# Performance work log

Measured on AMD Instinct MI355X. Metric: run time of the kernel, lower is better.

The kernel has to match this reference:

```python
import jax, jax.numpy as jnp
import numpy as np

B, L = 512, 260          # batch, raw input length
N_EMB, E_DIM = 8192, 128 * 65
NC = 16                   # num_classes


def setup_inputs() -> dict:
    key = jax.random.key(0)
    ks = jax.random.split(key, 12)
    rn = lambda k, shp, s: jax.random.normal(k, shp, jnp.float32) * s
    return {
        "x": rn(ks[0], (B, L), 1.0),
        # VQ codebook, init uniform(-1/K, 1/K) as in reference VQ-VAE
        "codebook": jax.random.uniform(ks[1], (N_EMB, E_DIM), jnp.float32, -1.0 / N_EMB, 1.0 / N_EMB),
        # encoder: Conv1d(1,64,k4,s2,p1) -> ReLU -> Conv1d(64,128,k4,s2,p1)
        "conv1_w": rn(ks[2], (64, 1, 4), 0.3), "conv1_b": jnp.zeros((64,), jnp.float32),
        "conv2_w": rn(ks[3], (128, 64, 4), 0.06), "conv2_b": jnp.zeros((128,), jnp.float32),
        # decoder: ConvT1d(128,64,k4,s2,p1) -> ReLU -> ConvT1d(64,1,k4,s2,p1); torch weight layout (in,out,k)
        "dec1_w": rn(ks[4], (128, 64, 4), 0.04), "dec1_b": jnp.zeros((64,), jnp.float32),
        "dec2_w": rn(ks[5], (64, 1, 4), 0.06), "dec2_b": jnp.zeros((1,), jnp.float32),
        # multitask head: Linear(4160, NC); torch layout (out,in)
        "mt_w": rn(ks[6], (NC, 4160), 0.015), "mt_b": jnp.zeros((NC,), jnp.float32),
        # adversary head: Linear(4160,256)->ReLU->Linear(256,128)->ReLU->Linear(128,NC)
        "adv_w1": rn(ks[7], (256, 4160), 0.015), "adv_b1": jnp.zeros((256,), jnp.float32),
        "adv_w2": rn(ks[8], (128, 256), 0.06), "adv_b2": jnp.zeros((128,), jnp.float32),
        "adv_w3": rn(ks[9], (NC, 128), 0.09), "adv_b3": jnp.zeros((NC,), jnp.float32),
        "beta": 0.25,
    }


def _conv1d(x, w, b, stride):
    # x: [B,C,L], w: [O,I,K] (torch Conv1d layout), padding=1
    y = jax.lax.conv_general_dilated(x, w, (stride,), [(1, 1)],
                                     dimension_numbers=("NCH", "OIH", "NCH"))
    return y + b[None, :, None]


def _convT1d(x, w, b, stride, k=4, p=1):
    # torch ConvTranspose1d(in,out,k,stride=s,padding=p); w: [I,O,K]
    # == dilated conv with lhs_dilation=s, padding=k-1-p, spatially-flipped, IO-swapped kernel
    wt = jnp.flip(w, -1).transpose(1, 0, 2)  # [O,I,K]
    pad = k - 1 - p
    y = jax.lax.conv_general_dilated(x, wt, (1,), [(pad, pad)], lhs_dilation=(stride,),
                                     dimension_numbers=("NCH", "OIH", "NCH"))
    return y + b[None, :, None]


def _forward(x, codebook, conv1_w, conv1_b, conv2_w, conv2_b,
             dec1_w, dec1_b, dec2_w, dec2_b, mt_w, mt_b,
             adv_w1, adv_b1, adv_w2, adv_b2, adv_w3, adv_b3, beta):
    sg = jax.lax.stop_gradient
    xb = x[:, None, :]                                      # x.unsqueeze_(1) -> [B,1,260]
    h = jax.nn.relu(_conv1d(xb, conv1_w, conv1_b, 2))       # [B,64,130]
    z_e = _conv1d(h, conv2_w, conv2_b, 2)                   # [B,128,65]
    b = z_e.shape[0]

    # ---- VectorQuantizer: cdist^2 / argmin / gather / commitment loss ----
    z = z_e.reshape(b, -1)                                  # [B,8320]
    d = (jnp.sum(z * z, axis=1, keepdims=True)
         + jnp.sum(codebook * codebook, axis=1)[None, :]
         - 2.0 * (z @ codebook.T))                          # [B,N_EMB]
    idx = jnp.argmin(d, axis=1)                             # [B]
    zq_raw = codebook[idx].reshape(z_e.shape)               # gather -> [B,128,65]
    emb_loss = (jnp.mean((sg(zq_raw) - z_e) ** 2)
                + beta * jnp.mean((zq_raw - sg(z_e)) ** 2))
    z_q = z_e + sg(zq_raw - z_e)                            # straight-through
    counts = jnp.zeros((codebook.shape[0],), z.dtype).at[idx].add(1.0)
    e_mean = counts / b
    perplexity = jnp.exp(-jnp.sum(e_mean * jnp.log(e_mean + 1e-10)))

    # ---- heads operate on z_e halves ----
    mt = z_e[:, :64, :].reshape(b, -1) @ mt_w.T + mt_b      # [B,NC]
    a = jax.nn.relu(z_e[:, 64:, :].reshape(b, -1) @ adv_w1.T + adv_b1)
    a = jax.nn.relu(a @ adv_w2.T + adv_b2)
    adv = a @ adv_w3.T + adv_b3                             # [B,NC]

    # ---- decoder on quantized codes ----
    hd = jax.nn.relu(_convT1d(z_q, dec1_w, dec1_b, 2))      # [B,64,130]
    x_hat = _convT1d(hd, dec2_w, dec2_b, 2)                 # [B,1,260]
    return emb_loss, x_hat, mt, adv, perplexity


def reference(x, codebook, conv1_w, conv1_b, conv2_w, conv2_b,
              dec1_w, dec1_b, dec2_w, dec2_b, mt_w, mt_b,
              adv_w1, adv_b1, adv_w2, adv_b2, adv_w3, adv_b3, beta):
    return _forward(x, codebook, conv1_w, conv1_b, conv2_w, conv2_b,
                    dec1_w, dec1_b, dec2_w, dec2_b, mt_w, mt_b,
                    adv_w1, adv_b1, adv_w2, adv_b2, adv_w3, adv_b3, beta)
```

## Files before the change

### kernel.cpp

```cpp
#include <hip/hip_runtime.h>
#include <stdint.h>

typedef __attribute__((ext_vector_type(8))) short s8v;
typedef __attribute__((ext_vector_type(4))) float f4v;

#define OUT_XHAT 1
#define OUT_MT   133121
#define OUT_ADV  141313
#define OUT_PERP 149505

#define WS_COUNTS   0
#define WS_EMB      8192
#define WS_A1       8256
#define WS_CN       139328
#define WS_ZN2      147520
#define WS_ZL1      148032
#define WS_CBL1     148544
#define WS_ZERO_N   156736
#define WS_ZE       156736
#define WS_SC0      4416576
#define WS_SC1      8610880
#define WS_HD       8676416
#define WS_W2T      12936256
#define WS_WE       12969024
#define WS_WO       12985408
#define WS_W2TA     13001792
#define WS_IDX      13034560
#define WS_ZPK      13035136
#define WS_CBT      15165056

__device__ __forceinline__ short f2bf(float f) {
  uint32_t u = __float_as_uint(f);
  u = (u + 0x7FFFu + ((u >> 16) & 1u)) >> 16;
  return (short)u;
}

__device__ __forceinline__ void gl_lds16(const void* g, void* l) {
  __builtin_amdgcn_global_load_lds(
      (const __attribute__((address_space(1))) void*)g,
      (__attribute__((address_space(3))) void*)l, 16, 0, 0);
}

__global__ void k_initprep(float* __restrict__ W, const float* __restrict__ c2w,
                           const float* __restrict__ d1w,
                           const float* __restrict__ aw2) {
  int id = blockIdx.x * 256 + threadIdx.x;
  if (id < WS_ZERO_N) W[id] = 0.f;
  float* w2t = W + WS_W2T;
  float* We = W + WS_WE;
  float* Wo = W + WS_WO;
  float* w2ta = W + WS_W2TA;
  if (id < 32768) {
    int c = id & 127, ik = id >> 7;
    int i = ik >> 2, k = ik & 3;
    w2t[id] = c2w[(c * 64 + i) * 4 + k];
    int kk = id >> 7;
    w2ta[id] = aw2[(id & 127) * 256 + kk];
  }
  if (id < 16384) {
    int o = id & 63, is = id >> 6;
    int i = is >> 1, s = is & 1;
    We[id] = d1w[(i * 64 + o) * 4 + (3 - 2 * s)];
    Wo[id] = d1w[(i * 64 + o) * 4 + (2 - 2 * s)];
  }
}

__device__ __forceinline__ void packmat_body(
    const float* __restrict__ src, short* __restrict__ dst,
    float* __restrict__ nrm2, float* __restrict__ l1, int R, int nb, int bid,
    int tid, short* tile, float* rsq, float* rl1) {
  int n0 = (bid % nb) * 64;
  int k0 = (bid / nb) * 64;
  int nr = tid >> 2, qc = tid & 3;
  const float* sp = src + (size_t)(n0 + nr) * 8320 + k0 + qc * 16;
  float v[16];
  *(float4*)&v[0] = *(const float4*)(sp);
  *(float4*)&v[4] = *(const float4*)(sp + 4);
  *(float4*)&v[8] = *(const float4*)(sp + 8);
  *(float4*)&v[12] = *(const float4*)(sp + 12);
  float sq = 0.f, sl = 0.f;
#pragma unroll
  for (int i = 0; i < 16; ++i) {
    sq = fmaf(v[i], v[i], sq);
    sl += fabsf(v[i]);
  }
  union { short s[8]; int4 q; } u0, u1;
#pragma unroll
  for (int j = 0; j < 8; ++j) {
    u0.s[j] = f2bf(v[j]);
    u1.s[j] = f2bf(v[8 + j]);
  }
  *(int4*)&tile[((qc * 2 + 0) * 64 + nr) * 8] = u0.q;
  *(int4*)&tile[((qc * 2 + 1) * 64 + nr) * 8] = u1.q;
  rsq[tid] = sq;
  rl1[tid] = sl;
  __syncthreads();
  if (tid < 64) {
    float s = rsq[tid * 4] + rsq[tid * 4 + 1] + rsq[tid * 4 + 2] + rsq[tid * 4 + 3];
    float t = rl1[tid * 4] + rl1[tid * 4 + 1] + rl1[tid * 4 + 2] + rl1[tid * 4 + 3];
    atomicAdd(&nrm2[n0 + tid], s);
    atomicAdd(&l1[n0 + tid], t);
  }
  int kc = tid >> 5, nn = (tid & 31) * 2;
  size_t ob = ((size_t)(k0 / 8 + kc) * R + n0 + nn) * 8;
  *(int4*)&dst[ob] = *(int4*)&tile[(kc * 64 + nn) * 8];
  *(int4*)&dst[ob + 8] = *(int4*)&tile[(kc * 64 + nn + 1) * 8];
}

__global__ __launch_bounds__(256) void k_megaA(
    const float* __restrict__ x, const float* __restrict__ c1w,
    const float* __restrict__ c1b, const float* __restrict__ w2t,
    const float* __restrict__ c2b, float* __restrict__ zebuf,
    const float* __restrict__ cb, short* __restrict__ cbt,
    float* __restrict__ cn, float* __restrict__ cbl1) {
  __shared__ __align__(16) char smem[28032];
  int bid = blockIdx.x, tid = threadIdx.x;
  if (bid < 520) {
    float* At = (float*)smem;
    float* Bt = At + 2048;
    float* xs = Bt + 4096;
    float* w1s = xs + 520;
    float* b1s = w1s + 256;
    int row0 = bid * 64;
    int tm = (tid & 15) * 4;
    int tn = (tid >> 4) * 8;
    int sr = tid & 63;
    int sj0 = (tid >> 6) * 8;
    int rowm = row0 + sr;
    int gb = rowm / 65;
    int gt = rowm - gb * 65;
    int gb0 = row0 / 65;
    int xrow = gb - gb0;
    int tpos = 2 * gt - 1;
    int bkr = tid >> 3;
    int bnc = (tid & 7) * 16;
    for (int u = tid; u < 520; u += 256) {
      int rr = gb0 + (u >= 260 ? 1 : 0);
      if (rr > 511) rr = 511;
      xs[u] = x[rr * 260 + (u >= 260 ? u - 260 : u)];
    }
    if (tid < 256) w1s[tid] = c1w[tid];
    if (tid < 64) b1s[tid] = c1b[tid];
    __syncthreads();
    float acc[4][8];
#pragma unroll
    for (int i = 0; i < 4; ++i)
#pragma unroll
      for (int j = 0; j < 8; ++j) acc[i][j] = 0.f;
    for (int k0i = 0; k0i < 256; k0i += 32) {
      float av[8];
#pragma unroll
      for (int u = 0; u < 8; ++u) {
        int jj = k0i + sj0 + u;
        int cc = jj >> 2;
        int kk = jj & 3;
        int p = tpos + kk;
        float hv = 0.f;
        if (p >= 0 && p < 130) {
          float a = b1s[cc];
          int base = 2 * p - 1;
#pragma unroll
          for (int k = 0; k < 4; ++k) {
            int xp = base + k;
            float xv = (xp >= 0 && xp < 260) ? xs[xrow * 260 + xp] : 0.f;
            a = fmaf(xv, w1s[cc * 4 + k], a);
          }
          hv = fmaxf(a, 0.f);
        }
        av[u] = hv;
      }
      float bvv[16];
#pragma unroll
      for (int u = 0; u < 16; ++u) bvv[u] = w2t[(k0i + bkr) * 128 + bnc + u];
      __syncthreads();
#pragma unroll
      for (int u = 0; u < 8; ++u) At[(sj0 + u) * 64 + sr] = av[u];
#pragma unroll
      for (int u = 0; u < 16; ++u) Bt[bkr * 128 + bnc + u] = bvv[u];
      __syncthreads();
#pragma unroll
      for (int kk = 0; kk < 32; ++kk) {
        float a0 = At[kk * 64 + tm + 0];
        float a1 = At[kk * 64 + tm + 1];
        float a2 = At[kk * 64 + tm + 2];
        float a3 = At[kk * 64 + tm + 3];
#pragma unroll
        for (int j = 0; j < 8; ++j) {
          float bv = Bt[kk * 128 + tn + j];
          acc[0][j] = fmaf(a0, bv, acc[0][j]);
          acc[1][j] = fmaf(a1, bv, acc[1][j]);
          acc[2][j] = fmaf(a2, bv, acc[2][j]);
          acc[3][j] = fmaf(a3, bv, acc[3][j]);
        }
      }
    }
#pragma unroll
    for (int i = 0; i < 4; ++i) {
      int rr = row0 + tm + i;
      int b = rr / 65, t = rr - b * 65;
#pragma unroll
      for (int j = 0; j < 8; ++j) {
        int n = tn + j;
        zebuf[(size_t)b * 8320 + (size_t)n * 65 + t] = acc[i][j] + c2b[n];
      }
    }
  } else {
    short* tile = (short*)smem;
    float* rsq = (float*)(smem + 8192);
    float* rl1 = rsq + 256;
    packmat_body(cb, cbt, cn, cbl1, 8192, 128, bid - 520, tid, tile, rsq, rl1);
  }
}

__global__ __launch_bounds__(256) void k_megaB(
    const float* __restrict__ z_e, const float* __restrict__ mtw,
    const float* __restrict__ mtb, const float* __restrict__ aw1,
    short* __restrict__ zpk, float* __restrict__ zn2, float* __restrict__ zl1,
    float* __restrict__ a1, float* __restrict__ out) {
  __shared__ __align__(16) char smem[16384];
  int bid = blockIdx.x, tid = threadIdx.x;
  if (bid < 320) {
    float* At = (float*)smem;
    float* Bt = At + 2048;
    int ksp = bid % 10;
    int nt = (bid / 10) & 3;
    int mt = bid / 40;
    int m0 = mt * 64, n0 = nt * 64, kb = ksp * 416;
    int tm = (tid & 15) * 4, tn = (tid >> 4) * 4;
    int sr = tid & 63, sj = (tid >> 6) * 8;
    const float* za = z_e + (size_t)(m0 + sr) * 8320 + 4160 + kb + sj;
    const float* wb = aw1 + (size_t)(n0 + sr) * 4160 + kb + sj;
    float acc[4][4];
#pragma unroll
    for (int i = 0; i < 4; ++i)
#pragma unroll
      for (int j = 0; j < 4; ++j) acc[i][j] = 0.f;
    for (int k0 = 0; k0 < 416; k0 += 32) {
      float4 av0 = *(const float4*)(za + k0);
      float4 av1 = *(const float4*)(za + k0 + 4);
      float4 bv0 = *(const float4*)(wb + k0);
      float4 bv1 = *(const float4*)(wb + k0 + 4);
      __syncthreads();
      At[(sj + 0) * 64 + sr] = av0.x; At[(sj + 1) * 64 + sr] = av0.y;
      At[(sj + 2) * 64 + sr] = av0.z; At[(sj + 3) * 64 + sr] = av0.w;
      At[(sj + 4) * 64 + sr] = av1.x; At[(sj + 5) * 64 + sr] = av1.y;
      At[(sj + 6) * 64 + sr] = av1.z; At[(sj + 7) * 64 + sr] = av1.w;
      Bt[(sj + 0) * 64 + sr] = bv0.x; Bt[(sj + 1) * 64 + sr] = bv0.y;
      Bt[(sj + 2) * 64 + sr] = bv0.z; Bt[(sj + 3) * 64 + sr] = bv0.w;
      Bt[(sj + 4) * 64 + sr] = bv1.x; Bt[(sj + 5) * 64 + sr] = bv1.y;
      Bt[(sj + 6) * 64 + sr] = bv1.z; Bt[(sj + 7) * 64 + sr] = bv1.w;
      __syncthreads();
#pragma unroll
      for (int kk = 0; kk < 32; ++kk) {
        float4 aa = *(const float4*)&At[kk * 64 + tm];
        float4 bb = *(const float4*)&Bt[kk * 64 + tn];
        acc[0][0] = fmaf(aa.x, bb.x, acc[0][0]); acc[0][1] = fmaf(aa.x, bb.y, acc[0][1]);
        acc[0][2] = fmaf(aa.x, bb.z, acc[0][2]); acc[0][3] = fmaf(aa.x, bb.w, acc[0][3]);
        acc[1][0] = fmaf(aa.y, bb.x, acc[1][0]); acc[1][1] = fmaf(aa.y, bb.y, acc[1][1]);
        acc[1][2] = fmaf(aa.y, bb.z, acc[1][2]); acc[1][3] = fmaf(aa.y, bb.w, acc[1][3]);
        acc[2][0] = fmaf(aa.z, bb.x, acc[2][0]); acc[2][1] = fmaf(aa.z, bb.y, acc[2][1]);
        acc[2][2] = fmaf(aa.z, bb.z, acc[2][2]); acc[2][3] = fmaf(aa.z, bb.w, acc[2][3]);
        acc[3][0] = fmaf(aa.w, bb.x, acc[3][0]); acc[3][1] = fmaf(aa.w, bb.y, acc[3][1]);
        acc[3][2] = fmaf(aa.w, bb.z, acc[3][2]); acc[3][3] = fmaf(aa.w, bb.w, acc[3][3]);
      }
    }
#pragma unroll
    for (int i = 0; i < 4; ++i)
#pragma unroll
      for (int j = 0; j < 4; ++j)
        atomicAdd(&a1[(size_t)(m0 + tm + i) * 256 + n0 + tn + j], acc[i][j]);
  } else if (bid < 832) {
    float* red = (float*)smem;
    int b = bid - 320;
    int wave = tid >> 6, lane = tid & 63;
    const float* zr = z_e + (size_t)b * 8320;
    float acc[16];
#pragma unroll
    for (int n = 0; n < 16; ++n) acc[n] = 0.f;
    for (int k4 = tid; k4 < 1040; k4 += 256) {
      float4 zv = *(const float4*)&zr[k4 * 4];
#pragma unroll
      for (int n = 0; n < 16; ++n) {
        float4 wv = *(const float4*)&mtw[n * 4160 + k4 * 4];
        float a = acc[n];
        a = fmaf(zv.x, wv.x, a);
        a = fmaf(zv.y, wv.y, a);
        a = fmaf(zv.z, wv.z, a);
        a = fmaf(zv.w, wv.w, a);
        acc[n] = a;
      }
    }
#pragma unroll
    for (int n = 0; n < 16; ++n) {
      float v = acc[n];
      for (int off = 32; off > 0; off >>= 1) v += __shfl_down(v, off);
      if (lane == 0) red[n * 4 + wave] = v;
    }
    __syncthreads();
    if (tid < 16) {
      float s = red[tid * 4] + red[tid * 4 + 1] + red[tid * 4 + 2] + red[tid * 4 + 3];
      out[OUT_MT + b * 16 + tid] = s + mtb[tid];
    }
  } else {
    short* tile = (short*)smem;
    float* rsq = (float*)(smem + 8192);
    float* rl1 = rsq + 256;
    packmat_body(z_e, zpk, zn2, zl1, 512, 8, bid - 832, tid, tile, rsq, rl1);
  }
}

__global__ __launch_bounds__(256) void k_scores(const short* __restrict__ cbt,
                                                const short* __restrict__ zpk,
                                                const float* __restrict__ cn,
                                                float* __restrict__ sc0,
                                                float* __restrict__ sc1) {
  __shared__ short As[8 * 128 * 8];
  __shared__ short Bs[8 * 128 * 8];
  int bid = blockIdx.x;
  int kh = bid & 1, nt = (bid >> 1) & 63, mt = bid >> 7;
  int tid = threadIdx.x;
  int wave = tid >> 6, lane = tid & 63;
  int q = lane >> 4, r16 = lane & 15;
  int m0 = mt * 128, n0 = nt * 128;
  int cb8 = kh * 520;
  int rb = (wave >> 1) * 64, cw = (wave & 1) * 64;

  f4v acc[4][4];
#pragma unroll
  for (int i = 0; i < 4; ++i)
#pragma unroll
    for (int j = 0; j < 4; ++j)
#pragma unroll
      for (int r = 0; r < 4; ++r) acc[i][j][r] = 0.f;

  for (int ks = 0; ks < 65; ++ks) {
    int c0 = cb8 + ks * 8;
    __syncthreads();
#pragma unroll
    for (int i = 0; i < 4; ++i) {
      int kc = wave * 2 + (i & 1);
      int h = (i >> 1) * 64;
      size_t gk = (size_t)(c0 + kc);
      gl_lds16(zpk + (gk * 512 + m0 + h + lane) * 8, &As[(kc * 128 + h) * 8]);
      gl_lds16(cbt + (gk * 8192 + n0 + h + lane) * 8, &Bs[(kc * 128 + h) * 8]);
    }
    __syncthreads();
    s8v af[2][4], bfr[2][4];
#pragma unroll
    for (int g = 0; g < 2; ++g) {
      int kq = (g * 4 + q) * 128;
#pragma unroll
      for (int i = 0; i < 4; ++i) {
        af[g][i] = *(const s8v*)&As[(kq + rb + i * 16 + r16) * 8];
        bfr[g][i] = *(const s8v*)&Bs[(kq + cw + i * 16 + r16) * 8];
      }
    }
#pragma unroll
    for (int g = 0; g < 2; ++g)
#pragma unroll
      for (int mi = 0; mi < 4; ++mi)
#pragma unroll
        for (int ni = 0; ni < 4; ++ni)
          acc[mi][ni] = __builtin_amdgcn_mfma_f32_16x16x32_bf16(
              af[g][mi], bfr[g][ni], acc[mi][ni], 0, 0, 0);
  }

  float* sc = kh ? sc1 : sc0;
#pragma unroll
  for (int mi = 0; mi < 4; ++mi) {
#pragma unroll
    for (int ni = 0; ni < 4; ++ni) {
      int col = n0 + cw + ni * 16 + r16;
      float cnv = kh ? 0.f : cn[col];
#pragma unroll
      for (int r = 0; r < 4; ++r) {
        int row = m0 + rb + mi * 16 + q * 4 + r;
        sc[(size_t)row * 8192 + col] = -2.f * acc[mi][ni][r] + cnv;
      }
    }
  }
}

__global__ __launch_bounds__(256) void k_argming(
    const float* __restrict__ s0, const float* __restrict__ s1,
    const float* __restrict__ z_e, const float* __restrict__ cb,
    const float* __restrict__ zn2, const float* __restrict__ cn,
    int* __restrict__ idx, float* __restrict__ counts,
    float* __restrict__ emb_acc) {
  __shared__ float srow[8192];
  __shared__ float red[256];
  __shared__ int cand[128];
  __shared__ float cval[128];
  __shared__ int ccnt;
  __shared__ int bsel;
  int b = blockIdx.x, tid = threadIdx.x;
  const float* r0 = s0 + (size_t)b * 8192;
  const float* r1 = s1 + (size_t)b * 8192;
  float mn = 1e30f;
  for (int j4 = tid; j4 < 2048; j4 += 256) {
    float4 a = *(const float4*)&r0[j4 * 4];
    float4 c = *(const float4*)&r1[j4 * 4];
    float4 v;
    v.x = a.x + c.x; v.y = a.y + c.y; v.z = a.z + c.z; v.w = a.w + c.w;
    *(float4*)&srow[j4 * 4] = v;
    mn = fminf(mn, fminf(fminf(v.x, v.y), fminf(v.z, v.w)));
  }
  red[tid] = mn;
  __syncthreads();
  for (int st = 128; st > 0; st >>= 1) {
    if (tid < st) red[tid] = fminf(red[tid], red[tid + st]);
    __syncthreads();
  }
  float minv = red[0];
  float margin = sqrtf(zn2[b]) * (1.0f / 131072.0f) + 1e-4f;
  if (tid == 0) ccnt = 0;
  __syncthreads();
  float thr = minv + margin;
  for (int j = tid; j < 8192; j += 256) {
    if (srow[j] <= thr) {
      int p = atomicAdd(&ccnt, 1);
      if (p < 128) cand[p] = j;
    }
  }
  __syncthreads();
  int nc = min(ccnt, 128);
  int wave = tid >> 6, lane = tid & 63;
  const float* zr = z_e + (size_t)b * 8320;
  float zn = zn2[b];
  for (int ci = wave; ci < nc; ci += 4) {
    int j = cand[ci];
    const float* cr = cb + (size_t)j * 8320;
    float dp = 0.f;
    for (int k4 = lane; k4 < 2080; k4 += 64) {
      float4 zv = *(const float4*)&zr[k4 * 4];
      float4 cv = *(const float4*)&cr[k4 * 4];
      dp = fmaf(zv.x, cv.x, dp);
      dp = fmaf(zv.y, cv.y, dp);
      dp = fmaf(zv.z, cv.z, dp);
      dp = fmaf(zv.w, cv.w, dp);
    }
    for (int off = 32; off > 0; off >>= 1) dp += __shfl_down(dp, off);
    if (lane == 0)
      cval[ci] = __fsub_rn(__fadd_rn(zn, cn[j]), __fmul_rn(2.f, dp));
  }
  __syncthreads();
  if (tid == 0) {
    float bv = 1e30f;
    int bj = 0x7fffffff;
    for (int ci = 0; ci < nc; ++ci) {
      float v = cval[ci];
      int j = cand[ci];
      if (v < bv || (v == bv && j < bj)) { bv = v; bj = j; }
    }
    idx[b] = bj;
    atomicAdd(&counts[bj], 1.0f);
    bsel = bj;
  }
  __syncthreads();
  int bj = bsel;
  const float* cr2 = cb + (size_t)bj * 8320;
  float part = 0.f;
  for (int k4 = tid; k4 < 2080; k4 += 256) {
    float4 cv = *(const float4*)&cr2[k4 * 4];
    float4 zv = *(const float4*)&zr[k4 * 4];
    float d0 = cv.x - zv.x, d1 = cv.y - zv.y;
    float d2 = cv.z - zv.z, d3 = cv.w - zv.w;
    part += d0 * d0 + d1 * d1 + d2 * d2 + d3 * d3;
  }
  red[tid] = part;
  __syncthreads();
  for (int st = 128; st > 0; st >>= 1) {
    if (tid < st) red[tid] += red[tid + st];
    __syncthreads();
  }
  if (tid == 0) atomicAdd(emb_acc, red[0]);
}

__global__ __launch_bounds__(256) void k_dec1both(
    const float* __restrict__ cb, const int* __restrict__ idxb,
    const float* __restrict__ We, const float* __restrict__ Wo,
    const float* __restrict__ bias, float* __restrict__ hd) {
  __shared__ float At[32 * 64];
  __shared__ float Bt[32 * 64];
  int bid = blockIdx.x, tid = threadIdx.x;
  int par = (bid >= 520) ? 1 : 0;
  int bl = bid - par * 520;
  const float* wt = par ? Wo : We;
  int toff = par - 1;
  int row0 = bl * 64;
  int tm = (tid & 15) * 4, tn = (tid >> 4) * 4;
  int sr = tid & 63, sj0 = (tid >> 6) * 8;
  int rowm = row0 + sr;
  int gb = rowm / 65, gt = rowm - gb * 65;
  const float* sbase = cb + (size_t)idxb[gb] * 8320;
  int tpos = gt + toff;
  int bkr = tid >> 3, bnc = (tid & 7) * 8;
  float acc[4][4];
#pragma unroll
  for (int i = 0; i < 4; ++i)
#pragma unroll
    for (int j = 0; j < 4; ++j) acc[i][j] = 0.f;
  for (int k0 = 0; k0 < 256; k0 += 32) {
    float av[8];
#pragma unroll
    for (int u = 0; u < 8; ++u) {
      int jj = k0 + sj0 + u;
      int cc = jj >> 1;
      int kk = jj & 1;
      int p = tpos + kk;
      av[u] = (p >= 0 && p < 65) ? sbase[cc * 65 + p] : 0.f;
    }
    float bvv[8];
#pragma unroll
    for (int u = 0; u < 8; ++u) bvv[u] = wt[(k0 + bkr) * 64 + bnc + u];
    __syncthreads();
#pragma unroll
    for (int u = 0; u < 8; ++u) At[(sj0 + u) * 64 + sr] = av[u];
#pragma unroll
    for (int u = 0; u < 8; ++u) Bt[bkr * 64 + bnc + u] = bvv[u];
    __syncthreads();
#pragma unroll
    for (int kk = 0; kk < 32; ++kk) {
      float a0 = At[kk * 64 + tm + 0];
      float a1 = At[kk * 64 + tm + 1];
      float a2 = At[kk * 64 + tm + 2];
      float a3 = At[kk * 64 + tm + 3];
#pragma unroll
      for (int j = 0; j < 4; ++j) {
        float bv = Bt[kk * 64 + tn + j];
        acc[0][j] = fmaf(a0, bv, acc[0][j]);
        acc[1][j] = fmaf(a1, bv, acc[1][j]);
        acc[2][j] = fmaf(a2, bv, acc[2][j]);
        acc[3][j] = fmaf(a3, bv, acc[3][j]);
      }
    }
  }
#pragma unroll
  for (int i = 0; i < 4; ++i) {
    int rr = row0 + tm + i;
    int b = rr / 65, t = rr - b * 65;
#pragma unroll
    for (int j = 0; j < 4; ++j) {
      int n = tn + j;
      float v = fmaxf(acc[i][j] + bias[n], 0.f);
      hd[(size_t)b * 8320 + (size_t)n * 130 + t * 2 + par] = v;
    }
  }
}

__global__ void k_megaC(const float* __restrict__ hd, const float* __restrict__ d2w,
                        const float* __restrict__ d2b,
                        const float* __restrict__ a1raw, const float* __restrict__ b1,
                        const float* __restrict__ w2ta, const float* __restrict__ b2,
                        const float* __restrict__ w3, const float* __restrict__ b3,
                        const float* __restrict__ counts,
                        const float* __restrict__ emb_acc,
                        const float* __restrict__ beta_p, float* __restrict__ out) {
  __shared__ float sbuf[384];
  int bid = blockIdx.x, tid = threadIdx.x;
  if (bid < 520) {
    int id = bid * 256 + tid;
    if (id >= 512 * 260) return;
    int b = id / 260, t = id % 260;
    int u = t >> 1;
    const float* hb = hd + (size_t)b * 8320;
    float acc = d2b[0];
    if (t & 1) {
      bool ok = (u + 1 < 130);
      for (int i = 0; i < 64; ++i) {
        acc = fmaf(hb[i * 130 + u], d2w[i * 4 + 2], acc);
        if (ok) acc = fmaf(hb[i * 130 + u + 1], d2w[i * 4 + 0], acc);
      }
    } else {
      bool ok = (u >= 1);
      for (int i = 0; i < 64; ++i) {
        if (ok) acc = fmaf(hb[i * 130 + u - 1], d2w[i * 4 + 3], acc);
        acc = fmaf(hb[i * 130 + u], d2w[i * 4 + 1], acc);
      }
    }
    out[OUT_XHAT + id] = acc;
  } else if (bid < 1032) {
    float* s1 = sbuf;
    float* s2 = sbuf + 256;
    int b = bid - 520;
    s1[tid] = fmaxf(a1raw[(size_t)b * 256 + tid] + b1[tid], 0.f);
    __syncthreads();
    if (tid < 128) {
      float acc = b2[tid];
      for (int k = 0; k < 256; ++k) acc = fmaf(s1[k], w2ta[k * 128 + tid], acc);
      s2[tid] = fmaxf(acc, 0.f);
    }
    __syncthreads();
    if (tid < 16) {
      float acc = b3[tid];
      for (int k = 0; k < 128; ++k) acc = fmaf(s2[k], w3[tid * 128 + k], acc);
      out[OUT_ADV + b * 16 + tid] = acc;
    }
  } else {
    float* red = sbuf;
    float part = 0.f;
    for (int j = tid; j < 8192; j += 256) {
      float e = counts[j] * (1.0f / 512.0f);
      part += e * logf(e + 1e-10f);
    }
    red[tid] = part;
    __syncthreads();
    for (int st = 128; st > 0; st >>= 1) {
      if (tid < st) red[tid] += red[tid + st];
      __syncthreads();
    }
    if (tid == 0) {
      out[OUT_PERP] = expf(-red[0]);
      out[0] = (1.f + beta_p[0]) * emb_acc[0] * (1.0f / 4259840.0f);
    }
  }
}

extern "C" void kernel_launch(void* const* d_in, const int* in_sizes, int n_in,
                              void* d_out, int out_size, void* d_ws, size_t ws_size,
                              hipStream_t stream) {
  (void)in_sizes; (void)n_in; (void)out_size; (void)ws_size;
  const float* x   = (const float*)d_in[0];
  const float* cb  = (const float*)d_in[1];
  const float* c1w = (const float*)d_in[2];
  const float* c1b = (const float*)d_in[3];
  const float* c2w = (const float*)d_in[4];
  const float* c2b = (const float*)d_in[5];
  const float* d1w = (const float*)d_in[6];
  const float* d1b = (const float*)d_in[7];
  const float* d2w = (const float*)d_in[8];
  const float* d2b = (const float*)d_in[9];
  const float* mtw = (const float*)d_in[10];
  const float* mtb = (const float*)d_in[11];
  const float* aw1 = (const float*)d_in[12];
  const float* ab1 = (const float*)d_in[13];
  const float* aw2 = (const float*)d_in[14];
  const float* ab2 = (const float*)d_in[15];
  const float* aw3 = (const float*)d_in[16];
  const float* ab3 = (const float*)d_in[17];
  const float* beta = (const float*)d_in[18];
  (void)aw2;
  float* out = (float*)d_out;
  float* W = (float*)d_ws;

  float* counts = W + WS_COUNTS;
  float* embac  = W + WS_EMB;
  float* a1buf  = W + WS_A1;
  float* cnbuf  = W + WS_CN;
  float* zn2    = W + WS_ZN2;
  float* zl1    = W + WS_ZL1;
  float* cbl1   = W + WS_CBL1;
  float* zebuf  = W + WS_ZE;
  float* sc0    = W + WS_SC0;
  float* sc1    = W + WS_SC1;
  float* hdbuf  = W + WS_HD;
  float* w2t    = W + WS_W2T;
  float* We     = W + WS_WE;
  float* Wo     = W + WS_WO;
  float* w2ta   = W + WS_W2TA;
  int*   idxb   = (int*)(W + WS_IDX);
  short* zpk    = (short*)(W + WS_ZPK);
  short* cbt    = (short*)(W + WS_CBT);

  k_initprep<<<613, 256, 0, stream>>>(W, c2w, d1w, aw2);
  k_megaA<<<520 + 16640, 256, 0, stream>>>(x, c1w, c1b, w2t, c2b, zebuf,
                                           cb, cbt, cnbuf, cbl1);
  k_megaB<<<320 + 512 + 1040, 256, 0, stream>>>(zebuf, mtw, mtb, aw1,
                                                zpk, zn2, zl1, a1buf, out);
  k_scores<<<512, 256, 0, stream>>>(cbt, zpk, cnbuf, sc0, sc1);
  k_argming<<<512, 256, 0, stream>>>(sc0, sc1, zebuf, cb, zn2, cnbuf, idxb,
                                     counts, embac);
  k_dec1both<<<1040, 256, 0, stream>>>(cb, idxb, We, Wo, d1b, hdbuf);
  k_megaC<<<520 + 512 + 1, 256, 0, stream>>>(hdbuf, d2w, d2b, a1buf, ab1,
                                             w2ta, ab2, aw3, ab3, counts,
                                             embac, beta, out);
}
```

Baseline: 703.2 us.

## Fuse codebook bf16 packing and norms into score GEMM, drop atomics

The separate pass that converts the 8192x8320 codebook to packed bf16 and computes its norms is removed. The score GEMM now loads fp32 codebook rows directly, converts them in registers with v_cvt_pk_bf16_f32, writes them to LDS, and prefetches the next k-slice. Codebook squared norms are accumulated only by the mt==0 blocks and written as per-half partials. Global atomics for the adversary partial sums, the code counts and the embedding loss are replaced by partial buffers and an in-block histogram, which also removes most of the workspace zeroing. The cost is that each of the 4 M-tiles now rereads and reconverts the fp32 codebook, and the B operand moves from async global-to-LDS copies to register staging.

```diff
diff --git a/kernel.cpp b/kernel.cpp
--- a/kernel.cpp
+++ b/kernel.cpp
@@ -9,25 +9,20 @@
 #define OUT_ADV  141313
 #define OUT_PERP 149505
 
-#define WS_COUNTS   0
-#define WS_EMB      8192
-#define WS_A1       8256
-#define WS_CN       139328
-#define WS_ZN2      147520
-#define WS_ZL1      148032
-#define WS_CBL1     148544
-#define WS_ZERO_N   156736
-#define WS_ZE       156736
-#define WS_SC0      4416576
-#define WS_SC1      8610880
-#define WS_HD       8676416
-#define WS_W2T      12936256
-#define WS_WE       12969024
-#define WS_WO       12985408
-#define WS_W2TA     13001792
-#define WS_IDX      13034560
-#define WS_ZPK      13035136
-#define WS_CBT      15165056
+#define WS_EMBP     0
+#define WS_A1P      512
+#define WS_CNP      1311232
+#define WS_ZN2      1327616
+#define WS_W2T      1328128
+#define WS_WE       1360896
+#define WS_WO       1377280
+#define WS_W2TA     1393664
+#define WS_IDX      1426432
+#define WS_ZE       1426944
+#define WS_SC0      5686784
+#define WS_SC1      9881088
+#define WS_HD       14075392
+#define WS_ZPK      18335232
 
 __device__ __forceinline__ short f2bf(float f) {
   uint32_t u = __float_as_uint(f);
@@ -35,6 +30,12 @@
   return (short)u;
 }
 
+__device__ __forceinline__ uint32_t cvtpk(float a, float b) {
+  uint32_t r;
+  asm("v_cvt_pk_bf16_f32 %0, %1, %2" : "=v"(r) : "v"(a), "v"(b));
+  return r;
+}
+
 __device__ __forceinline__ void gl_lds16(const void* g, void* l) {
   __builtin_amdgcn_global_load_lds(
       (const __attribute__((address_space(1))) void*)g,
@@ -45,11 +46,11 @@
                            const float* __restrict__ d1w,
                            const float* __restrict__ aw2) {
   int id = blockIdx.x * 256 + threadIdx.x;
-  if (id < WS_ZERO_N) W[id] = 0.f;
   float* w2t = W + WS_W2T;
   float* We = W + WS_WE;
   float* Wo = W + WS_WO;
   float* w2ta = W + WS_W2TA;
+  if (id < 512) (W + WS_ZN2)[id] = 0.f;
   if (id < 32768) {
     int c = id & 127, ik = id >> 7;
     int i = ik >> 2, k = ik & 3;
@@ -65,12 +66,106 @@
   }
 }
 
-__device__ __forceinline__ void packmat_body(
+__global__ __launch_bounds__(256) void k_conv2f(
+    const float* __restrict__ x, const float* __restrict__ c1w,
+    const float* __restrict__ c1b, const float* __restrict__ w2t,
+    const float* __restrict__ c2b, float* __restrict__ zebuf) {
+  __shared__ float At[32 * 64];
+  __shared__ float Bt[32 * 128];
+  __shared__ float xs[520];
+  __shared__ float w1s[256];
+  __shared__ float b1s[64];
+  int bid = blockIdx.x, tid = threadIdx.x;
+  int row0 = bid * 64;
+  int tm = (tid & 15) * 4;
+  int tn = (tid >> 4) * 8;
+  int sr = tid & 63;
+  int sj0 = (tid >> 6) * 8;
+  int rowm = row0 + sr;
+  int gb = rowm / 65;
+  int gt = rowm - gb * 65;
+  int gb0 = row0 / 65;
+  int xrow = gb - gb0;
+  int tpos = 2 * gt - 1;
+  int bkr = tid >> 3;
+  int bnc = (tid & 7) * 16;
+  for (int u = tid; u < 520; u += 256) {
+    int rr = gb0 + (u >= 260 ? 1 : 0);
+    if (rr > 511) rr = 511;
+    xs[u] = x[rr * 260 + (u >= 260 ? u - 260 : u)];
+  }
+  if (tid < 256) w1s[tid] = c1w[tid];
+  if (tid < 64) b1s[tid] = c1b[tid];
+  __syncthreads();
+  float acc[4][8];
+#pragma unroll
+  for (int i = 0; i < 4; ++i)
+#pragma unroll
+    for (int j = 0; j < 8; ++j) acc[i][j] = 0.f;
+  for (int k0i = 0; k0i < 256; k0i += 32) {
+    float av[8];
+#pragma unroll
+    for (int u = 0; u < 8; ++u) {
+      int jj = k0i + sj0 + u;
+      int cc = jj >> 2;
+      int kk = jj & 3;
+      int p = tpos + kk;
+      float hv = 0.f;
+      if (p >= 0 && p < 130) {
+        float a = b1s[cc];
+        int base = 2 * p - 1;
+#pragma unroll
+        for (int k = 0; k < 4; ++k) {
+          int xp = base + k;
+          float xv = (xp >= 0 && xp < 260) ? xs[xrow * 260 + xp] : 0.f;
+          a = fmaf(xv, w1s[cc * 4 + k], a);
+        }
+        hv = fmaxf(a, 0.f);
+      }
+      av[u] = hv;
+    }
+    float bvv[16];
+#pragma unroll
+    for (int u = 0; u < 16; ++u) bvv[u] = w2t[(k0i + bkr) * 128 + bnc + u];
+    __syncthreads();
+#pragma unroll
+    for (int u = 0; u < 8; ++u) At[(sj0 + u) * 64 + sr] = av[u];
+#pragma unroll
+    for (int u = 0; u < 16; ++u) Bt[bkr * 128 + bnc + u] = bvv[u];
+    __syncthreads();
+#pragma unroll
+    for (int kk = 0; kk < 32; ++kk) {
+      float a0 = At[kk * 64 + tm + 0];
+      float a1 = At[kk * 64 + tm + 1];
+      float a2 = At[kk * 64 + tm + 2];
+      float a3 = At[kk * 64 + tm + 3];
+#pragma unroll
+      for (int j = 0; j < 8; ++j) {
+        float bv = Bt[kk * 128 + tn + j];
+        acc[0][j] = fmaf(a0, bv, acc[0][j]);
+        acc[1][j] = fmaf(a1, bv, acc[1][j]);
+        acc[2][j] = fmaf(a2, bv, acc[2][j]);
+        acc[3][j] = fmaf(a3, bv, acc[3][j]);
+      }
+    }
+  }
+#pragma unroll
+  for (int i = 0; i < 4; ++i) {
+    int rr = row0 + tm + i;
+    int b = rr / 65, t = rr - b * 65;
+#pragma unroll
+    for (int j = 0; j < 8; ++j) {
+      int n = tn + j;
+      zebuf[(size_t)b * 8320 + (size_t)n * 65 + t] = acc[i][j] + c2b[n];
+    }
+  }
+}
+
+__device__ __forceinline__ void packz_body(
     const float* __restrict__ src, short* __restrict__ dst,
-    float* __restrict__ nrm2, float* __restrict__ l1, int R, int nb, int bid,
-    int tid, short* tile, float* rsq, float* rl1) {
-  int n0 = (bid % nb) * 64;
-  int k0 = (bid / nb) * 64;
+    float* __restrict__ nrm2, int bid, int tid, short* tile, float* rsq) {
+  int n0 = (bid % 8) * 64;
+  int k0 = (bid / 8) * 64;
   int nr = tid >> 2, qc = tid & 3;
   const float* sp = src + (size_t)(n0 + nr) * 8320 + k0 + qc * 16;
   float v[16];
@@ -78,12 +173,9 @@
   *(float4*)&v[4] = *(const float4*)(sp + 4);
   *(float4*)&v[8] = *(const float4*)(sp + 8);
   *(float4*)&v[12] = *(const float4*)(sp + 12);
-  float sq = 0.f, sl = 0.f;
-#pragma unroll
-  for (int i = 0; i < 16; ++i) {
-    sq = fmaf(v[i], v[i], sq);
-    sl += fabsf(v[i]);
-  }
+  float sq = 0.f;
+#pragma unroll
+  for (int i = 0; i < 16; ++i) sq = fmaf(v[i], v[i], sq);
   union { short s[8]; int4 q; } u0, u1;
 #pragma unroll
   for (int j = 0; j < 8; ++j) {
@@ -93,130 +185,22 @@
   *(int4*)&tile[((qc * 2 + 0) * 64 + nr) * 8] = u0.q;
   *(int4*)&tile[((qc * 2 + 1) * 64 + nr) * 8] = u1.q;
   rsq[tid] = sq;
-  rl1[tid] = sl;
   __syncthreads();
   if (tid < 64) {
     float s = rsq[tid * 4] + rsq[tid * 4 + 1] + rsq[tid * 4 + 2] + rsq[tid * 4 + 3];
-    float t = rl1[tid * 4] + rl1[tid * 4 + 1] + rl1[tid * 4 + 2] + rl1[tid * 4 + 3];
     atomicAdd(&nrm2[n0 + tid], s);
-    atomicAdd(&l1[n0 + tid], t);
   }
   int kc = tid >> 5, nn = (tid & 31) * 2;
-  size_t ob = ((size_t)(k0 / 8 + kc) * R + n0 + nn) * 8;
+  size_t ob = ((size_t)(k0 / 8 + kc) * 512 + n0 + nn) * 8;
   *(int4*)&dst[ob] = *(int4*)&tile[(kc * 64 + nn) * 8];
   *(int4*)&dst[ob + 8] = *(int4*)&tile[(kc * 64 + nn + 1) * 8];
-}
-
-__global__ __launch_bounds__(256) void k_megaA(
-    const float* __restrict__ x, const float* __restrict__ c1w,
-    const float* __restrict__ c1b, const float* __restrict__ w2t,
-    const float* __restrict__ c2b, float* __restrict__ zebuf,
-    const float* __restrict__ cb, short* __restrict__ cbt,
-    float* __restrict__ cn, float* __restrict__ cbl1) {
-  __shared__ __align__(16) char smem[28032];
-  int bid = blockIdx.x, tid = threadIdx.x;
-  if (bid < 520) {
-    float* At = (float*)smem;
-    float* Bt = At + 2048;
-    float* xs = Bt + 4096;
-    float* w1s = xs + 520;
-    float* b1s = w1s + 256;
-    int row0 = bid * 64;
-    int tm = (tid & 15) * 4;
-    int tn = (tid >> 4) * 8;
-    int sr = tid & 63;
-    int sj0 = (tid >> 6) * 8;
-    int rowm = row0 + sr;
-    int gb = rowm / 65;
-    int gt = rowm - gb * 65;
-    int gb0 = row0 / 65;
-    int xrow = gb - gb0;
-    int tpos = 2 * gt - 1;
-    int bkr = tid >> 3;
-    int bnc = (tid & 7) * 16;
-    for (int u = tid; u < 520; u += 256) {
-      int rr = gb0 + (u >= 260 ? 1 : 0);
-      if (rr > 511) rr = 511;
-      xs[u] = x[rr * 260 + (u >= 260 ? u - 260 : u)];
-    }
-    if (tid < 256) w1s[tid] = c1w[tid];
-    if (tid < 64) b1s[tid] = c1b[tid];
-    __syncthreads();
-    float acc[4][8];
-#pragma unroll
-    for (int i = 0; i < 4; ++i)
-#pragma unroll
-      for (int j = 0; j < 8; ++j) acc[i][j] = 0.f;
-    for (int k0i = 0; k0i < 256; k0i += 32) {
-      float av[8];
-#pragma unroll
-      for (int u = 0; u < 8; ++u) {
-        int jj = k0i + sj0 + u;
-        int cc = jj >> 2;
-        int kk = jj & 3;
-        int p = tpos + kk;
-        float hv = 0.f;
-        if (p >= 0 && p < 130) {
-          float a = b1s[cc];
-          int base = 2 * p - 1;
-#pragma unroll
-          for (int k = 0; k < 4; ++k) {
-            int xp = base + k;
-            float xv = (xp >= 0 && xp < 260) ? xs[xrow * 260 + xp] : 0.f;
-            a = fmaf(xv, w1s[cc * 4 + k], a);
-          }
-          hv = fmaxf(a, 0.f);
-        }
-        av[u] = hv;
-      }
-      float bvv[16];
-#pragma unroll
-      for (int u = 0; u < 16; ++u) bvv[u] = w2t[(k0i + bkr) * 128 + bnc + u];
-      __syncthreads();
-#pragma unroll
-      for (int u = 0; u < 8; ++u) At[(sj0 + u) * 64 + sr] = av[u];
-#pragma unroll
-      for (int u = 0; u < 16; ++u) Bt[bkr * 128 + bnc + u] = bvv[u];
-      __syncthreads();
-#pragma unroll
-      for (int kk = 0; kk < 32; ++kk) {
-        float a0 = At[kk * 64 + tm + 0];
-        float a1 = At[kk * 64 + tm + 1];
-        float a2 = At[kk * 64 + tm + 2];
-        float a3 = At[kk * 64 + tm + 3];
-#pragma unroll
-        for (int j = 0; j < 8; ++j) {
-          float bv = Bt[kk * 128 + tn + j];
-          acc[0][j] = fmaf(a0, bv, acc[0][j]);
-          acc[1][j] = fmaf(a1, bv, acc[1][j]);
-          acc[2][j] = fmaf(a2, bv, acc[2][j]);
-          acc[3][j] = fmaf(a3, bv, acc[3][j]);
-        }
-      }
-    }
-#pragma unroll
-    for (int i = 0; i < 4; ++i) {
-      int rr = row0 + tm + i;
-      int b = rr / 65, t = rr - b * 65;
-#pragma unroll
-      for (int j = 0; j < 8; ++j) {
-        int n = tn + j;
-        zebuf[(size_t)b * 8320 + (size_t)n * 65 + t] = acc[i][j] + c2b[n];
-      }
-    }
-  } else {
-    short* tile = (short*)smem;
-    float* rsq = (float*)(smem + 8192);
-    float* rl1 = rsq + 256;
-    packmat_body(cb, cbt, cn, cbl1, 8192, 128, bid - 520, tid, tile, rsq, rl1);
-  }
 }
 
 __global__ __launch_bounds__(256) void k_megaB(
     const float* __restrict__ z_e, const float* __restrict__ mtw,
     const float* __restrict__ mtb, const float* __restrict__ aw1,
-    short* __restrict__ zpk, float* __restrict__ zn2, float* __restrict__ zl1,
-    float* __restrict__ a1, float* __restrict__ out) {
+    short* __restrict__ zpk, float* __restrict__ zn2,
+    float* __restrict__ a1p, float* __restrict__ out) {
   __shared__ __align__(16) char smem[16384];
   int bid = blockIdx.x, tid = threadIdx.x;
   if (bid < 320) {
@@ -268,7 +252,7 @@
     for (int i = 0; i < 4; ++i)
 #pragma unroll
       for (int j = 0; j < 4; ++j)
-        atomicAdd(&a1[(size_t)(m0 + tm + i) * 256 + n0 + tn + j], acc[i][j]);
+        a1p[((size_t)ksp * 512 + m0 + tm + i) * 256 + n0 + tn + j] = acc[i][j];
   } else if (bid < 832) {
     float* red = (float*)smem;
     int b = bid - 320;
@@ -304,16 +288,14 @@
   } else {
     short* tile = (short*)smem;
     float* rsq = (float*)(smem + 8192);
-    float* rl1 = rsq + 256;
-    packmat_body(z_e, zpk, zn2, zl1, 512, 8, bid - 832, tid, tile, rsq, rl1);
-  }
-}
-
-__global__ __launch_bounds__(256) void k_scores(const short* __restrict__ cbt,
-                                                const short* __restrict__ zpk,
-                                                const float* __restrict__ cn,
-                                                float* __restrict__ sc0,
-                                                float* __restrict__ sc1) {
+    packz_body(z_e, zpk, zn2, bid - 832, tid, tile, rsq);
+  }
+}
+
+__global__ __launch_bounds__(256, 2) void k_scores(
+    const float* __restrict__ cb, const short* __restrict__ zpk,
+    float* __restrict__ sc0, float* __restrict__ sc1,
+    float* __restrict__ cnp) {
   __shared__ short As[8 * 128 * 8];
   __shared__ short Bs[8 * 128 * 8];
   int bid = blockIdx.x;
@@ -324,6 +306,9 @@
   int m0 = mt * 128, n0 = nt * 128;
   int cb8 = kh * 520;
   int rb = (wave >> 1) * 64, cw = (wave & 1) * 64;
+  int bn = tid >> 1, bkq = (tid & 1) * 32;
+  const float* brow = cb + (size_t)(n0 + bn) * 8320 + kh * 4160 + bkq;
+  short* bdst = &Bs[((bkq >> 3) * 128 + bn) * 8];
 
   f4v acc[4][4];
 #pragma unroll
@@ -332,9 +317,41 @@
     for (int j = 0; j < 4; ++j)
 #pragma unroll
       for (int r = 0; r < 4; ++r) acc[i][j][r] = 0.f;
+
+  float csq = 0.f;
+  const float4* bp = (const float4*)brow;
+  float4 f0 = bp[0], f1 = bp[1], f2 = bp[2], f3 = bp[3];
+  float4 f4_ = bp[4], f5 = bp[5], f6 = bp[6], f7 = bp[7];
 
   for (int ks = 0; ks < 65; ++ks) {
     int c0 = cb8 + ks * 8;
+    if (mt == 0) {
+      csq = fmaf(f0.x, f0.x, csq); csq = fmaf(f0.y, f0.y, csq);
+      csq = fmaf(f0.z, f0.z, csq); csq = fmaf(f0.w, f0.w, csq);
+      csq = fmaf(f1.x, f1.x, csq); csq = fmaf(f1.y, f1.y, csq);
+      csq = fmaf(f1.z, f1.z, csq); csq = fmaf(f1.w, f1.w, csq);
+      csq = fmaf(f2.x, f2.x, csq); csq = fmaf(f2.y, f2.y, csq);
+      csq = fmaf(f2.z, f2.z, csq); csq = fmaf(f2.w, f2.w, csq);
+      csq = fmaf(f3.x, f3.x, csq); csq = fmaf(f3.y, f3.y, csq);
+      csq = fmaf(f3.z, f3.z, csq); csq = fmaf(f3.w, f3.w, csq);
+      csq = fmaf(f4_.x, f4_.x, csq); csq = fmaf(f4_.y, f4_.y, csq);
+      csq = fmaf(f4_.z, f4_.z, csq); csq = fmaf(f4_.w, f4_.w, csq);
+      csq = fmaf(f5.x, f5.x, csq); csq = fmaf(f5.y, f5.y, csq);
+      csq = fmaf(f5.z, f5.z, csq); csq = fmaf(f5.w, f5.w, csq);
+      csq = fmaf(f6.x, f6.x, csq); csq = fmaf(f6.y, f6.y, csq);
+      csq = fmaf(f6.z, f6.z, csq); csq = fmaf(f6.w, f6.w, csq);
+      csq = fmaf(f7.x, f7.x, csq); csq = fmaf(f7.y, f7.y, csq);
+      csq = fmaf(f7.z, f7.z, csq); csq = fmaf(f7.w, f7.w, csq);
+    }
+    int4 w0, w1, w2, w3;
+    w0.x = (int)cvtpk(f0.x, f0.y); w0.y = (int)cvtpk(f0.z, f0.w);
+    w0.z = (int)cvtpk(f1.x, f1.y); w0.w = (int)cvtpk(f1.z, f1.w);
+    w1.x = (int)cvtpk(f2.x, f2.y); w1.y = (int)cvtpk(f2.z, f2.w);
+    w1.z = (int)cvtpk(f3.x, f3.y); w1.w = (int)cvtpk(f3.z, f3.w);
+    w2.x = (int)cvtpk(f4_.x, f4_.y); w2.y = (int)cvtpk(f4_.z, f4_.w);
+    w2.z = (int)cvtpk(f5.x, f5.y); w2.w = (int)cvtpk(f5.z, f5.w);
+    w3.x = (int)cvtpk(f6.x, f6.y); w3.y = (int)cvtpk(f6.z, f6.w);
+    w3.z = (int)cvtpk(f7.x, f7.y); w3.w = (int)cvtpk(f7.z, f7.w);
     __syncthreads();
 #pragma unroll
     for (int i = 0; i < 4; ++i) {
@@ -342,9 +359,17 @@
       int h = (i >> 1) * 64;
       size_t gk = (size_t)(c0 + kc);
       gl_lds16(zpk + (gk * 512 + m0 + h + lane) * 8, &As[(kc * 128 + h) * 8]);
-      gl_lds16(cbt + (gk * 8192 + n0 + h + lane) * 8, &Bs[(kc * 128 + h) * 8]);
-    }
-    __syncthreads();
+    }
+    *(int4*)(bdst + 0 * 128 * 8) = w0;
+    *(int4*)(bdst + 1 * 128 * 8) = w1;
+    *(int4*)(bdst + 2 * 128 * 8) = w2;
+    *(int4*)(bdst + 3 * 128 * 8) = w3;
+    __syncthreads();
+    if (ks < 64) {
+      const float4* np = (const float4*)(brow + (ks + 1) * 64);
+      f0 = np[0]; f1 = np[1]; f2 = np[2]; f3 = np[3];
+      f4_ = np[4]; f5 = np[5]; f6 = np[6]; f7 = np[7];
+    }
     s8v af[2][4], bfr[2][4];
 #pragma unroll
     for (int g = 0; g < 2; ++g) {
@@ -365,17 +390,20 @@
               af[g][mi], bfr[g][ni], acc[mi][ni], 0, 0, 0);
   }
 
+  if (mt == 0) {
+    csq += __shfl_xor(csq, 1);
+    if (!(tid & 1)) cnp[kh * 8192 + n0 + bn] = csq;
+  }
   float* sc = kh ? sc1 : sc0;
 #pragma unroll
   for (int mi = 0; mi < 4; ++mi) {
 #pragma unroll
     for (int ni = 0; ni < 4; ++ni) {
       int col = n0 + cw + ni * 16 + r16;
-      float cnv = kh ? 0.f : cn[col];
 #pragma unroll
       for (int r = 0; r < 4; ++r) {
         int row = m0 + rb + mi * 16 + q * 4 + r;
-        sc[(size_t)row * 8192 + col] = -2.f * acc[mi][ni][r] + cnv;
+        sc[(size_t)row * 8192 + col] = -2.f * acc[mi][ni][r];
       }
     }
   }
@@ -384,9 +412,8 @@
 __global__ __launch_bounds__(256) void k_argming(
     const float* __restrict__ s0, const float* __restrict__ s1,
     const float* __restrict__ z_e, const float* __restrict__ cb,
-    const float* __restrict__ zn2, const float* __restrict__ cn,
-    int* __restrict__ idx, float* __restrict__ counts,
-    float* __restrict__ emb_acc) {
+    const float* __restrict__ zn2, const float* __restrict__ cnp,
+    int* __restrict__ idx, float* __restrict__ embp) {
   __shared__ float srow[8192];
   __shared__ float red[256];
   __shared__ int cand[128];
@@ -396,12 +423,19 @@
   int b = blockIdx.x, tid = threadIdx.x;
   const float* r0 = s0 + (size_t)b * 8192;
   const float* r1 = s1 + (size_t)b * 8192;
+  const float* cn0 = cnp;
+  const float* cn1 = cnp + 8192;
   float mn = 1e30f;
   for (int j4 = tid; j4 < 2048; j4 += 256) {
     float4 a = *(const float4*)&r0[j4 * 4];
     float4 c = *(const float4*)&r1[j4 * 4];
+    float4 n = *(const float4*)&cn0[j4 * 4];
+    float4 m2 = *(const float4*)&cn1[j4 * 4];
     float4 v;
-    v.x = a.x + c.x; v.y = a.y + c.y; v.z = a.z + c.z; v.w = a.w + c.w;
+    v.x = a.x + c.x + (n.x + m2.x);
+    v.y = a.y + c.y + (n.y + m2.y);
+    v.z = a.z + c.z + (n.z + m2.z);
+    v.w = a.w + c.w + (n.w + m2.w);
     *(float4*)&srow[j4 * 4] = v;
     mn = fminf(mn, fminf(fminf(v.x, v.y), fminf(v.z, v.w)));
   }
@@ -440,8 +474,10 @@
       dp = fmaf(zv.w, cv.w, dp);
     }
     for (int off = 32; off > 0; off >>= 1) dp += __shfl_down(dp, off);
-    if (lane == 0)
-      cval[ci] = __fsub_rn(__fadd_rn(zn, cn[j]), __fmul_rn(2.f, dp));
+    if (lane == 0) {
+      float cnj = __fadd_rn(cn0[j], cn1[j]);
+      cval[ci] = __fsub_rn(__fadd_rn(zn, cnj), __fmul_rn(2.f, dp));
+    }
   }
   __syncthreads();
   if (tid == 0) {
@@ -453,7 +489,6 @@
       if (v < bv || (v == bv && j < bj)) { bv = v; bj = j; }
     }
     idx[b] = bj;
-    atomicAdd(&counts[bj], 1.0f);
     bsel = bj;
   }
   __syncthreads();
@@ -473,7 +508,7 @@
     if (tid < st) red[tid] += red[tid + st];
     __syncthreads();
   }
-  if (tid == 0) atomicAdd(emb_acc, red[0]);
+  if (tid == 0) embp[b] = red[0];
 }
 
 __global__ __launch_bounds__(256) void k_dec1both(
@@ -550,12 +585,13 @@
 
 __global__ void k_megaC(const float* __restrict__ hd, const float* __restrict__ d2w,
                         const float* __restrict__ d2b,
-                        const float* __restrict__ a1raw, const float* __restrict__ b1,
+                        const float* __restrict__ a1p, const float* __restrict__ b1,
                         const float* __restrict__ w2ta, const float* __restrict__ b2,
                         const float* __restrict__ w3, const float* __restrict__ b3,
-                        const float* __restrict__ counts,
-                        const float* __restrict__ emb_acc,
+                        const int* __restrict__ idxb,
+                        const float* __restrict__ embp,
                         const float* __restrict__ beta_p, float* __restrict__ out) {
+  __shared__ int hsh[8192];
   __shared__ float sbuf[384];
   int bid = blockIdx.x, tid = threadIdx.x;
   if (bid < 520) {
@@ -583,7 +619,11 @@
     float* s1 = sbuf;
     float* s2 = sbuf + 256;
     int b = bid - 520;
-    s1[tid] = fmaxf(a1raw[(size_t)b * 256 + tid] + b1[tid], 0.f);
+    float s = b1[tid];
+    const float* ap = a1p + (size_t)b * 256 + tid;
+#pragma unroll
+    for (int p = 0; p < 10; ++p) s += ap[(size_t)p * 131072];
+    s1[tid] = fmaxf(s, 0.f);
     __syncthreads();
     if (tid < 128) {
       float acc = b2[tid];
@@ -598,20 +638,34 @@
     }
   } else {
     float* red = sbuf;
+    for (int j = tid; j < 8192; j += 256) hsh[j] = 0;
+    __syncthreads();
+    for (int i = tid; i < 512; i += 256) atomicAdd(&hsh[idxb[i]], 1);
+    __syncthreads();
     float part = 0.f;
     for (int j = tid; j < 8192; j += 256) {
-      float e = counts[j] * (1.0f / 512.0f);
+      float e = (float)hsh[j] * (1.0f / 512.0f);
       part += e * logf(e + 1e-10f);
     }
+    float ep = 0.f;
+    for (int i = tid; i < 512; i += 256) ep += embp[i];
     red[tid] = part;
     __syncthreads();
     for (int st = 128; st > 0; st >>= 1) {
       if (tid < st) red[tid] += red[tid + st];
       __syncthreads();
     }
+    float negH = red[0];
+    __syncthreads();
+    red[tid] = ep;
+    __syncthreads();
+    for (int st = 128; st > 0; st >>= 1) {
+      if (tid < st) red[tid] += red[tid + st];
+      __syncthreads();
+    }
     if (tid == 0) {
-      out[OUT_PERP] = expf(-red[0]);
-      out[0] = (1.f + beta_p[0]) * emb_acc[0] * (1.0f / 4259840.0f);
+      out[OUT_PERP] = expf(-negH);
+      out[0] = (1.f + beta_p[0]) * red[0] * (1.0f / 4259840.0f);
     }
   }
 }
@@ -639,39 +693,32 @@
   const float* aw3 = (const float*)d_in[16];
   const float* ab3 = (const float*)d_in[17];
   const float* beta = (const float*)d_in[18];
-  (void)aw2;
   float* out = (float*)d_out;
   float* W = (float*)d_ws;
 
-  float* counts = W + WS_COUNTS;
-  float* embac  = W + WS_EMB;
-  float* a1buf  = W + WS_A1;
-  float* cnbuf  = W + WS_CN;
+  float* embp   = W + WS_EMBP;
+  float* a1p    = W + WS_A1P;
+  float* cnp    = W + WS_CNP;
   float* zn2    = W + WS_ZN2;
-  float* zl1    = W + WS_ZL1;
-  float* cbl1   = W + WS_CBL1;
-  float* zebuf  = W + WS_ZE;
-  float* sc0    = W + WS_SC0;
-  float* sc1    = W + WS_SC1;
-  float* hdbuf  = W + WS_HD;
   float* w2t    = W + WS_W2T;
   float* We     = W + WS_WE;
   float* Wo     = W + WS_WO;
   float* w2ta   = W + WS_W2TA;
   int*   idxb   = (int*)(W + WS_IDX);
+  float* zebuf  = W + WS_ZE;
+  float* sc0    = W + WS_SC0;
+  float* sc1    = W + WS_SC1;
+  float* hdbuf  = W + WS_HD;
   short* zpk    = (short*)(W + WS_ZPK);
-  short* cbt    = (short*)(W + WS_CBT);
-
-  k_initprep<<<613, 256, 0, stream>>>(W, c2w, d1w, aw2);
-  k_megaA<<<520 + 16640, 256, 0, stream>>>(x, c1w, c1b, w2t, c2b, zebuf,
-                                           cb, cbt, cnbuf, cbl1);
+
+  k_initprep<<<128, 256, 0, stream>>>(W, c2w, d1w, aw2);
+  k_conv2f<<<520, 256, 0, stream>>>(x, c1w, c1b, w2t, c2b, zebuf);
   k_megaB<<<320 + 512 + 1040, 256, 0, stream>>>(zebuf, mtw, mtb, aw1,
-                                                zpk, zn2, zl1, a1buf, out);
-  k_scores<<<512, 256, 0, stream>>>(cbt, zpk, cnbuf, sc0, sc1);
-  k_argming<<<512, 256, 0, stream>>>(sc0, sc1, zebuf, cb, zn2, cnbuf, idxb,
-                                     counts, embac);
+                                                zpk, zn2, a1p, out);
+  k_scores<<<512, 256, 0, stream>>>(cb, zpk, sc0, sc1, cnp);
+  k_argming<<<512, 256, 0, stream>>>(sc0, sc1, zebuf, cb, zn2, cnp, idxb, embp);
   k_dec1both<<<1040, 256, 0, stream>>>(cb, idxb, We, Wo, d1b, hdbuf);
-  k_megaC<<<520 + 512 + 1, 256, 0, stream>>>(hdbuf, d2w, d2b, a1buf, ab1,
-                                             w2ta, ab2, aw3, ab3, counts,
-                                             embac, beta, out);
-}
+  k_megaC<<<520 + 512 + 1, 256, 0, stream>>>(hdbuf, d2w, d2b, a1p, ab1,
+                                             w2ta, ab2, aw3, ab3, idxb,
+                                             embp, beta, out);
+}
```

Result: slower. 739.9 us (+5.2%).
